# Optimization experiments

Hardware: AMD Instinct MI355X
Metric: run time of the kernel (lower is better)

## Reference

```python
import jax, jax.numpy as jnp
import numpy as np

B, T, D, H, E = 4, 2048, 1024, 4096, 8


def setup_inputs() -> dict:
    key = jax.random.key(0)
    ks = jax.random.split(key, 7)
    x = jax.random.normal(ks[0], (B, T, D), dtype=jnp.float32)
    # Gate: Linear(D, E)
    Wg = jax.random.normal(ks[1], (D, E), dtype=jnp.float32) / np.sqrt(D)
    bg = jax.random.normal(ks[2], (E,), dtype=jnp.float32) * 0.01
    # Experts: E x [Linear(D,H), ReLU, Linear(H,D)] (dropout inactive at eval)
    W1 = jax.random.normal(ks[3], (E, D, H), dtype=jnp.float32) / np.sqrt(D)
    b1 = jax.random.normal(ks[4], (E, H), dtype=jnp.float32) * 0.01
    W2 = jax.random.normal(ks[5], (E, H, D), dtype=jnp.float32) / np.sqrt(H)
    b2 = jax.random.normal(ks[6], (E, D), dtype=jnp.float32) * 0.01
    return {"x": x, "Wg": Wg, "bg": bg, "W1": W1, "b1": b1, "W2": W2, "b2": b2}


def reference(x, Wg, bg, W1, b1, W2, b2):
    # Gate + hard top-1 routing
    gate_scores = x @ Wg + bg                      # [B,T,E]
    top1 = jnp.argmax(gate_scores, axis=-1)        # [B,T]
    onehot = jax.nn.one_hot(top1, Wg.shape[-1], dtype=x.dtype)  # [B,T,E]
    # Dense: every expert MLP over all tokens (matches original's masked
    # formulation: x*mask == x on selected tokens, output re-masked).
    h = jax.nn.relu(jnp.einsum('btd,edh->beth', x, W1) + b1[None, :, None, :])
    y = jnp.einsum('beth,ehd->betd', h, W2) + b2[None, :, None, :]
    # Masked combine: keep only the token's chosen expert output
    out = jnp.einsum('betd,bte->btd', y, onehot)
    return out
```

## Files before the change

kernel.cpp:

```cpp
#include <hip/hip_runtime.h>
#include <hip/hip_bf16.h>
#include <stdint.h>

#define NTOK 8192
#define DDIM 1024
#define HDIM 4096
#define NEXP 8
#define MAXWL1 48
#define MAXWL2 72
#define FFN1_GRID ((HDIM / 128) * MAXWL1)

typedef __attribute__((ext_vector_type(4))) float f32x4;
typedef __attribute__((ext_vector_type(8))) short s16x8;
typedef __attribute__((ext_vector_type(8))) unsigned short u16x8;

__device__ __forceinline__ unsigned short f2bf(float f) {
  union { float f; unsigned int u; } v; v.f = f;
  unsigned int u = v.u;
  u += 0x7FFFu + ((u >> 16) & 1u);
  return (unsigned short)(u >> 16);
}

typedef __attribute__((address_space(3))) unsigned char lds_u8;
typedef const __attribute__((address_space(1))) unsigned char glb_u8;

__device__ __forceinline__ void load_lds16(const void* g, void* l) {
  __builtin_amdgcn_global_load_lds((glb_u8*)g, (lds_u8*)l, 16, 0, 0);
}

__global__ __launch_bounds__(256) void gate_kernel(
    const float* __restrict__ x, const float* __restrict__ Wg,
    const float* __restrict__ bg, int* __restrict__ counts,
    int* __restrict__ lists) {
  const int lane = threadIdx.x & 63;
  const int tok = blockIdx.x * 4 + (threadIdx.x >> 6);
  const float* xr = x + (size_t)tok * DDIM;
  double acc[NEXP];
#pragma unroll
  for (int e = 0; e < NEXP; ++e) acc[e] = 0.0;
#pragma unroll 4
  for (int it = 0; it < DDIM / 64; ++it) {
    const int d = it * 64 + lane;
    const float xv = xr[d];
    const f32x4 w0 = *(const f32x4*)(Wg + (size_t)d * NEXP);
    const f32x4 w1 = *(const f32x4*)(Wg + (size_t)d * NEXP + 4);
#pragma unroll
    for (int j = 0; j < 4; ++j) {
      acc[j]     += (double)xv * (double)w0[j];
      acc[4 + j] += (double)xv * (double)w1[j];
    }
  }
#pragma unroll
  for (int e = 0; e < NEXP; ++e) {
    double v = acc[e];
#pragma unroll
    for (int off = 32; off > 0; off >>= 1) v += __shfl_xor(v, off, 64);
    acc[e] = v;
  }
  if (lane == 0) {
    int best = 0;
    double bv = acc[0] + (double)bg[0];
#pragma unroll
    for (int e = 1; e < NEXP; ++e) {
      const double v = acc[e] + (double)bg[e];
      if (v > bv) { bv = v; best = e; }
    }
    const int pos = atomicAdd(&counts[best], 1);
    lists[best * NTOK + pos] = tok;
  }
}

__global__ void offs_kernel(const int* __restrict__ counts, int* __restrict__ offs,
                            int* __restrict__ wl1, int* __restrict__ wl2) {
  int s = 0;
#pragma unroll
  for (int e = 0; e < NEXP; ++e) { offs[e] = s; s += counts[e]; }
  offs[NEXP] = s;
  int n1 = 0, n2 = 0;
  for (int e = 0; e < NEXP; ++e) {
    const int nb1 = (counts[e] + 255) >> 8;
    for (int b = 0; b < nb1; ++b) wl1[n1++] = (e << 20) | b;
    const int nb2 = (counts[e] + 127) >> 7;
    for (int b = 0; b < nb2; ++b) wl2[n2++] = (e << 20) | b;
  }
  offs[NEXP + 1] = n1;
  offs[NEXP + 2] = n2;
}

__device__ __forceinline__ void transpose_tile(
    const float* __restrict__ ine, unsigned short* __restrict__ oute,
    int R, int C, int c0, int r0, int t, unsigned short* Tb) {
  const int tr = t >> 4, tc4 = (t & 15) * 4;
#pragma unroll
  for (int p = 0; p < 4; ++p) {
    const int r = tr + p * 16;
    const f32x4 v = *(const f32x4*)(ine + (size_t)(r0 + r) * C + c0 + tc4);
#pragma unroll
    for (int j = 0; j < 4; ++j) Tb[r * 66 + tc4 + j] = f2bf(v[j]);
  }
  __syncthreads();
  const int cc = t >> 3, rr8 = (t & 7) * 8;
#pragma unroll
  for (int p = 0; p < 2; ++p) {
    const int c = cc + p * 32;
    u16x8 o;
#pragma unroll
    for (int j = 0; j < 8; ++j) o[j] = Tb[(rr8 + j) * 66 + c];
    *(u16x8*)(oute + (size_t)(c0 + c) * R + r0 + rr8) = o;
  }
}

__global__ __launch_bounds__(256) void transpose_conv_kernel(
    const float* __restrict__ in, unsigned short* __restrict__ out,
    int R, int C) {
  __shared__ __align__(16) unsigned short T[64 * 66];
  const int e = blockIdx.z;
  transpose_tile(in + (size_t)e * R * C, out + (size_t)e * C * R, R, C,
                 blockIdx.x * 64, blockIdx.y * 64, threadIdx.x, T);
}

__global__ __launch_bounds__(512) void gather_w1t_kernel(
    const float* __restrict__ x, const int* __restrict__ offs,
    const int* __restrict__ lists, int* __restrict__ stok,
    unsigned short* __restrict__ xbs, const float* __restrict__ W1,
    unsigned short* __restrict__ Wt1) {
  __shared__ __align__(16) unsigned short TT[2][64 * 66];
  const int bid = blockIdx.x;
  const int tid = threadIdx.x;
  if (bid < NTOK / 8) {
    const int p = bid * 8 + (tid >> 6);
    const int lane = tid & 63;
    int e = 0;
#pragma unroll
    for (int k = 1; k < NEXP; ++k) e += (p >= offs[k]) ? 1 : 0;
    const int tok = lists[e * NTOK + (p - offs[e])];
    if (lane == 0) stok[p] = tok;
    const float* src = x + (size_t)tok * DDIM + lane * 16;
    unsigned short* dst = xbs + (size_t)p * DDIM + lane * 16;
#pragma unroll
    for (int q = 0; q < 2; ++q) {
      const f32x4 a = *(const f32x4*)(src + q * 8);
      const f32x4 b = *(const f32x4*)(src + q * 8 + 4);
      u16x8 o;
#pragma unroll
      for (int j = 0; j < 4; ++j) { o[j] = f2bf(a[j]); o[4 + j] = f2bf(b[j]); }
      *(u16x8*)(dst + q * 8) = o;
    }
  } else {
    const int id = (bid - NTOK / 8) * 2 + (tid >> 8);
    const int t = tid & 255;
    const int e = id >> 10, rem = id & 1023;
    const int cb = rem & 63, rb = rem >> 6;
    transpose_tile(W1 + (size_t)e * DDIM * HDIM, Wt1 + (size_t)e * HDIM * DDIM,
                   DDIM, HDIM, cb * 64, rb * 64, t, TT[tid >> 8]);
  }
}

template <int BM, int BN, int WM, int WN, int K, int N, int MAXWLT,
          bool COLFAST, bool FUSE1>
__device__ __forceinline__ void ffn_body(
    int d, const unsigned short* __restrict__ A,
    const unsigned short* __restrict__ Bt, const float* __restrict__ bias,
    const int* __restrict__ counts, const int* __restrict__ offs,
    const int* __restrict__ wl, const int* __restrict__ stok,
    unsigned short* __restrict__ outb, float* __restrict__ outf, int nwl_idx,
    unsigned short* As0, unsigned short* Bs0,
    unsigned short* As1, unsigned short* Bs1) {
  constexpr int MF = BM / (WM * 16);
  constexpr int NF = BN / (WN * 16);
  constexpr int ISS_A = BM / 128;
  constexpr int ISS_B = BN / 128;
  constexpr int NT = K / 32;
  constexpr int NCB = N / BN;
  constexpr int NWG = NCB * MAXWLT;
  static_assert((NWG & 7) == 0 && (NT & 1) == 0 && NT >= 4, "");
  static_assert(WM * WN == 8, "8 waves");

  const int logical = (d & 7) * (NWG / 8) + (d >> 3);
  int cb, wli;
  if constexpr (COLFAST) { cb = logical % NCB; wli = logical / NCB; }
  else                   { cb = logical / MAXWLT; wli = logical % MAXWLT; }
  if (wli >= offs[nwl_idx]) return;
  const int col0 = cb * BN;
  const int wle = wl[wli];
  const int e = wle >> 20;
  const int bx = wle & 0xFFFFF;
  const int cnt = counts[e];
  const int row0 = offs[e] + bx * BM;

  const int tid = threadIdx.x;
  const int lane = tid & 63;
  const int w = tid >> 6;
  const int wm = w / WN;
  const int wn = w % WN;
  const int fr = lane & 15;
  const int fj = lane >> 4;

  const int swsrc = ((tid & 3) ^ ((tid >> 3) & 3)) * 8;
  const int rb = tid >> 2;
  const unsigned short* srcA[ISS_A];
#pragma unroll
  for (int i = 0; i < ISS_A; ++i) {
    int gr = row0 + i * 128 + rb;
    if (gr > NTOK - 1) gr = NTOK - 1;
    srcA[i] = A + (size_t)gr * K + swsrc;
  }
  const unsigned short* Bte = Bt + (size_t)e * N * K;
  const unsigned short* srcB[ISS_B];
#pragma unroll
  for (int i = 0; i < ISS_B; ++i)
    srcB[i] = Bte + (size_t)(col0 + i * 128 + rb) * K + swsrc;

  const int js = (fj ^ ((fr >> 1) & 3)) * 8;

  f32x4 acc[MF][NF];
#pragma unroll
  for (int m = 0; m < MF; ++m)
#pragma unroll
    for (int n = 0; n < NF; ++n) acc[m][n] = f32x4{0.f, 0.f, 0.f, 0.f};

  auto stage = [&](unsigned short* dA, unsigned short* dB, int kel) {
#pragma unroll
    for (int i = 0; i < ISS_A; ++i)
      load_lds16(srcA[i] + kel, dA + i * 4096 + tid * 8);
#pragma unroll
    for (int i = 0; i < ISS_B; ++i)
      load_lds16(srcB[i] + kel, dB + i * 4096 + tid * 8);
  };

  auto phase = [&](const unsigned short* pA, const unsigned short* pB,
                   unsigned short* nA, unsigned short* nB, int knext,
                   bool do_stage) {
    asm volatile("s_waitcnt vmcnt(0)" ::: "memory");
    __builtin_amdgcn_s_barrier();
    asm volatile("" ::: "memory");
    s16x8 af[MF], bf[NF];
#pragma unroll
    for (int m = 0; m < MF; ++m)
      af[m] = *(const s16x8*)(pA + (wm * MF * 16 + m * 16 + fr) * 32 + js);
#pragma unroll
    for (int n = 0; n < NF; ++n)
      bf[n] = *(const s16x8*)(pB + (wn * NF * 16 + n * 16 + fr) * 32 + js);
    if (do_stage) stage(nA, nB, knext);
    __builtin_amdgcn_s_setprio(1);
#pragma unroll
    for (int m = 0; m < MF; ++m)
#pragma unroll
      for (int n = 0; n < NF; ++n)
        acc[m][n] = __builtin_amdgcn_mfma_f32_16x16x32_bf16(af[m], bf[n],
                                                            acc[m][n], 0, 0, 0);
    __builtin_amdgcn_s_setprio(0);
  };

  stage(As0, Bs0, 0);
#pragma unroll 1
  for (int t = 0; t < NT - 2; t += 2) {
    phase(As0, Bs0, As1, Bs1, (t + 1) * 32, true);
    phase(As1, Bs1, As0, Bs0, (t + 2) * 32, true);
  }
  phase(As0, Bs0, As1, Bs1, (NT - 1) * 32, true);
  phase(As1, Bs1, nullptr, nullptr, 0, false);

#pragma unroll
  for (int n = 0; n < NF; ++n) {
    const int col = col0 + wn * NF * 16 + n * 16 + fr;
    const float bv = bias[e * N + col];
#pragma unroll
    for (int m = 0; m < MF; ++m) {
#pragma unroll
      for (int j = 0; j < 4; ++j) {
        const int rl = wm * MF * 16 + m * 16 + fj * 4 + j;
        if (bx * BM + rl < cnt) {
          if constexpr (FUSE1) {
            outb[(size_t)(row0 + rl) * N + col] = f2bf(fmaxf(acc[m][n][j] + bv, 0.f));
          } else {
            outf[(size_t)stok[row0 + rl] * N + col] = acc[m][n][j] + bv;
          }
        }
      }
    }
  }
}

__global__ __launch_bounds__(512, 4) void ffn1_w2t_kernel(
    const unsigned short* __restrict__ A, const unsigned short* __restrict__ Bt,
    const float* __restrict__ bias, const int* __restrict__ counts,
    const int* __restrict__ offs, const int* __restrict__ wl,
    const int* __restrict__ stok, unsigned short* __restrict__ Hs,
    const float* __restrict__ W2, unsigned short* __restrict__ Wt2) {
  __shared__ __align__(16) unsigned short As0[256 * 32], Bs0[128 * 32];
  __shared__ __align__(16) unsigned short As1[256 * 32], Bs1[128 * 32];
  const int bid = blockIdx.x;
  if (bid < FFN1_GRID) {
    ffn_body<256, 128, 4, 2, DDIM, HDIM, MAXWL1, false, true>(
        bid, A, Bt, bias, counts, offs, wl, stok, Hs, nullptr, NEXP + 1,
        As0, Bs0, As1, Bs1);
  } else {
    const int id = (bid - FFN1_GRID) * 2 + (threadIdx.x >> 8);
    const int t = threadIdx.x & 255;
    const int e = id >> 10, rem = id & 1023;
    const int cb = rem & 15, rb = rem >> 4;
    transpose_tile(W2 + (size_t)e * HDIM * DDIM, Wt2 + (size_t)e * DDIM * HDIM,
                   HDIM, DDIM, cb * 64, rb * 64, t,
                   (threadIdx.x >= 256) ? As1 : As0);
  }
}

template <int BM, int BN, int WM, int WN, int K, int N, int MAXWLT,
          bool COLFAST, bool FUSE1>
__global__ __launch_bounds__(512, 4) void ffn_kernel(
    const unsigned short* __restrict__ A, const unsigned short* __restrict__ Bt,
    const float* __restrict__ bias, const int* __restrict__ counts,
    const int* __restrict__ offs, const int* __restrict__ wl,
    const int* __restrict__ stok, unsigned short* __restrict__ outb,
    float* __restrict__ outf, int nwl_idx) {
  __shared__ __align__(16) unsigned short As0[BM * 32], Bs0[BN * 32];
  __shared__ __align__(16) unsigned short As1[BM * 32], Bs1[BN * 32];
  ffn_body<BM, BN, WM, WN, K, N, MAXWLT, COLFAST, FUSE1>(
      blockIdx.x, A, Bt, bias, counts, offs, wl, stok, outb, outf, nwl_idx,
      As0, Bs0, As1, Bs1);
}

extern "C" void kernel_launch(void* const* d_in, const int* in_sizes, int n_in,
                              void* d_out, int out_size, void* d_ws, size_t ws_size,
                              hipStream_t stream) {
  (void)in_sizes; (void)n_in; (void)out_size;
  const float* x  = (const float*)d_in[0];
  const float* Wg = (const float*)d_in[1];
  const float* bg = (const float*)d_in[2];
  const float* W1 = (const float*)d_in[3];
  const float* b1 = (const float*)d_in[4];
  const float* W2 = (const float*)d_in[5];
  const float* b2 = (const float*)d_in[6];
  float* out = (float*)d_out;

  char* ws = (char*)d_ws;
  const size_t OFF_CNT = 0;
  const size_t OFF_OFF = 128;
  const size_t OFF_WL1 = 256;
  const size_t OFF_WL2 = 256 + MAXWL1 * 4;
  const size_t OFF_LST = 1024;
  const size_t OFF_STK = OFF_LST + (size_t)NEXP * NTOK * 4;
  const size_t OFF_XBS = OFF_STK + (size_t)NTOK * 4;
  const size_t OFF_HS  = OFF_XBS + (size_t)NTOK * DDIM * 2;
  const size_t OFF_WT1 = OFF_HS + (size_t)NTOK * HDIM * 2;
  const size_t SZ_W    = (size_t)NEXP * DDIM * HDIM * 2;
  const size_t OFF_WT2 = OFF_WT1 + SZ_W;
  const size_t NEED_SMALL = OFF_WT1 + SZ_W;
  const size_t NEED_BIG   = OFF_WT2 + SZ_W;
  if (ws_size < NEED_SMALL) return;
  const bool big = (ws_size >= NEED_BIG);

  int* counts = (int*)(ws + OFF_CNT);
  int* offs   = (int*)(ws + OFF_OFF);
  int* wl1    = (int*)(ws + OFF_WL1);
  int* wl2    = (int*)(ws + OFF_WL2);
  int* lists  = (int*)(ws + OFF_LST);
  int* stok   = (int*)(ws + OFF_STK);
  unsigned short* xbs = (unsigned short*)(ws + OFF_XBS);
  unsigned short* Hs  = (unsigned short*)(ws + OFF_HS);
  unsigned short* Wt1 = (unsigned short*)(ws + OFF_WT1);
  unsigned short* Wt2 = big ? (unsigned short*)(ws + OFF_WT2) : Wt1;

  hipMemsetAsync(counts, 0, 128, stream);
  gate_kernel<<<NTOK / 4, 256, 0, stream>>>(x, Wg, bg, counts, lists);
  offs_kernel<<<1, 1, 0, stream>>>(counts, offs, wl1, wl2);

  gather_w1t_kernel<<<NTOK / 8 + 4096, 512, 0, stream>>>(
      x, offs, lists, stok, xbs, W1, Wt1);

  if (big) {
    ffn1_w2t_kernel<<<FFN1_GRID + 4096, 512, 0, stream>>>(
        xbs, Wt1, b1, counts, offs, wl1, stok, Hs, W2, Wt2);
  } else {
    ffn_kernel<256, 128, 4, 2, DDIM, HDIM, MAXWL1, false, true>
        <<<dim3(FFN1_GRID), 512, 0, stream>>>(
            xbs, Wt1, b1, counts, offs, wl1, stok, Hs, nullptr, NEXP + 1);
    transpose_conv_kernel<<<dim3(DDIM / 64, HDIM / 64, NEXP), 256, 0, stream>>>(
        W2, Wt1, HDIM, DDIM);
  }
  ffn_kernel<128, 256, 2, 4, HDIM, DDIM, MAXWL2, true, false>
      <<<dim3((DDIM / 256) * MAXWL2), 512, 0, stream>>>(
          Hs, Wt2, b2, counts, offs, wl2, stok, nullptr, out, NEXP + 2);
}
```

Baseline: 434.0 us.

## Fuse gate routing with W1 transpose and compute offsets in last gate block

Moves the gate computation into the same launch as the W1 transpose/bf16 conversion, so routing overlaps with the weight conversion instead of running as its own kernel. The offsets and worklists are built by whichever gate block finishes last, using an atomic completion counter, which removes the single-thread offs kernel launch. The token gather and bf16 conversion move into a separate kernel after that launch. This trades two small launches for one extra gather launch, and it relies on atomic-counter ordering across blocks being visible without an explicit memory fence.

```diff
diff --git a/kernel.cpp b/kernel.cpp
--- a/kernel.cpp
+++ b/kernel.cpp
@@ -9,6 +9,7 @@
 #define MAXWL1 48
 #define MAXWL2 72
 #define FFN1_GRID ((HDIM / 128) * MAXWL1)
+#define NGATE (NTOK / 8)
 
 typedef __attribute__((ext_vector_type(4))) float f32x4;
 typedef __attribute__((ext_vector_type(8))) short s16x8;
@@ -28,12 +29,10 @@
   __builtin_amdgcn_global_load_lds((glb_u8*)g, (lds_u8*)l, 16, 0, 0);
 }
 
-__global__ __launch_bounds__(256) void gate_kernel(
+__device__ __forceinline__ void gate_wave(
     const float* __restrict__ x, const float* __restrict__ Wg,
     const float* __restrict__ bg, int* __restrict__ counts,
-    int* __restrict__ lists) {
-  const int lane = threadIdx.x & 63;
-  const int tok = blockIdx.x * 4 + (threadIdx.x >> 6);
+    int* __restrict__ lists, int tok, int lane) {
   const float* xr = x + (size_t)tok * DDIM;
   double acc[NEXP];
 #pragma unroll
@@ -70,21 +69,38 @@
   }
 }
 
-__global__ void offs_kernel(const int* __restrict__ counts, int* __restrict__ offs,
-                            int* __restrict__ wl1, int* __restrict__ wl2) {
+__global__ __launch_bounds__(256) void gate_kernel(
+    const float* __restrict__ x, const float* __restrict__ Wg,
+    const float* __restrict__ bg, int* __restrict__ counts,
+    int* __restrict__ lists) {
+  gate_wave(x, Wg, bg, counts, lists, blockIdx.x * 4 + (threadIdx.x >> 6),
+            threadIdx.x & 63);
+}
+
+__device__ __forceinline__ void compute_offs(
+    const int* cnt, int* __restrict__ offs, int* __restrict__ wl1,
+    int* __restrict__ wl2) {
   int s = 0;
 #pragma unroll
-  for (int e = 0; e < NEXP; ++e) { offs[e] = s; s += counts[e]; }
+  for (int e = 0; e < NEXP; ++e) { offs[e] = s; s += cnt[e]; }
   offs[NEXP] = s;
   int n1 = 0, n2 = 0;
   for (int e = 0; e < NEXP; ++e) {
-    const int nb1 = (counts[e] + 255) >> 8;
+    const int nb1 = (cnt[e] + 255) >> 8;
     for (int b = 0; b < nb1; ++b) wl1[n1++] = (e << 20) | b;
-    const int nb2 = (counts[e] + 127) >> 7;
+    const int nb2 = (cnt[e] + 127) >> 7;
     for (int b = 0; b < nb2; ++b) wl2[n2++] = (e << 20) | b;
   }
   offs[NEXP + 1] = n1;
   offs[NEXP + 2] = n2;
+}
+
+__global__ void offs_kernel(const int* __restrict__ counts, int* __restrict__ offs,
+                            int* __restrict__ wl1, int* __restrict__ wl2) {
+  int c[NEXP];
+#pragma unroll
+  for (int e = 0; e < NEXP; ++e) c[e] = counts[e];
+  compute_offs(c, offs, wl1, wl2);
 }
 
 __device__ __forceinline__ void transpose_tile(
@@ -119,40 +135,58 @@
                  blockIdx.x * 64, blockIdx.y * 64, threadIdx.x, T);
 }
 
-__global__ __launch_bounds__(512) void gather_w1t_kernel(
-    const float* __restrict__ x, const int* __restrict__ offs,
-    const int* __restrict__ lists, int* __restrict__ stok,
-    unsigned short* __restrict__ xbs, const float* __restrict__ W1,
-    unsigned short* __restrict__ Wt1) {
+__global__ __launch_bounds__(512) void gate_w1t_kernel(
+    const float* __restrict__ x, const float* __restrict__ Wg,
+    const float* __restrict__ bg, int* __restrict__ counts,
+    int* __restrict__ lists, int* __restrict__ doneCnt,
+    int* __restrict__ offs, int* __restrict__ wl1, int* __restrict__ wl2,
+    const float* __restrict__ W1, unsigned short* __restrict__ Wt1) {
   __shared__ __align__(16) unsigned short TT[2][64 * 66];
   const int bid = blockIdx.x;
   const int tid = threadIdx.x;
-  if (bid < NTOK / 8) {
-    const int p = bid * 8 + (tid >> 6);
-    const int lane = tid & 63;
-    int e = 0;
-#pragma unroll
-    for (int k = 1; k < NEXP; ++k) e += (p >= offs[k]) ? 1 : 0;
-    const int tok = lists[e * NTOK + (p - offs[e])];
-    if (lane == 0) stok[p] = tok;
-    const float* src = x + (size_t)tok * DDIM + lane * 16;
-    unsigned short* dst = xbs + (size_t)p * DDIM + lane * 16;
-#pragma unroll
-    for (int q = 0; q < 2; ++q) {
-      const f32x4 a = *(const f32x4*)(src + q * 8);
-      const f32x4 b = *(const f32x4*)(src + q * 8 + 4);
-      u16x8 o;
-#pragma unroll
-      for (int j = 0; j < 4; ++j) { o[j] = f2bf(a[j]); o[4 + j] = f2bf(b[j]); }
-      *(u16x8*)(dst + q * 8) = o;
+  if (bid < NGATE) {
+    gate_wave(x, Wg, bg, counts, lists, bid * 8 + (tid >> 6), tid & 63);
+    __syncthreads();
+    if (tid == 0) {
+      const int d = atomicAdd(doneCnt, 1);
+      if (d == NGATE - 1) {
+        int c[NEXP];
+#pragma unroll
+        for (int e = 0; e < NEXP; ++e) c[e] = atomicAdd(&counts[e], 0);
+        compute_offs(c, offs, wl1, wl2);
+      }
     }
   } else {
-    const int id = (bid - NTOK / 8) * 2 + (tid >> 8);
+    const int id = (bid - NGATE) * 2 + (tid >> 8);
     const int t = tid & 255;
     const int e = id >> 10, rem = id & 1023;
     const int cb = rem & 63, rb = rem >> 6;
     transpose_tile(W1 + (size_t)e * DDIM * HDIM, Wt1 + (size_t)e * HDIM * DDIM,
                    DDIM, HDIM, cb * 64, rb * 64, t, TT[tid >> 8]);
+  }
+}
+
+__global__ __launch_bounds__(256) void gather_conv_kernel(
+    const float* __restrict__ x, const int* __restrict__ offs,
+    const int* __restrict__ lists, int* __restrict__ stok,
+    unsigned short* __restrict__ xbs) {
+  const int p = blockIdx.x * 4 + (threadIdx.x >> 6);
+  const int lane = threadIdx.x & 63;
+  int e = 0;
+#pragma unroll
+  for (int k = 1; k < NEXP; ++k) e += (p >= offs[k]) ? 1 : 0;
+  const int tok = lists[e * NTOK + (p - offs[e])];
+  if (lane == 0) stok[p] = tok;
+  const float* src = x + (size_t)tok * DDIM + lane * 16;
+  unsigned short* dst = xbs + (size_t)p * DDIM + lane * 16;
+#pragma unroll
+  for (int q = 0; q < 2; ++q) {
+    const f32x4 a = *(const f32x4*)(src + q * 8);
+    const f32x4 b = *(const f32x4*)(src + q * 8 + 4);
+    u16x8 o;
+#pragma unroll
+    for (int j = 0; j < 4; ++j) { o[j] = f2bf(a[j]); o[4 + j] = f2bf(b[j]); }
+    *(u16x8*)(dst + q * 8) = o;
   }
 }
 
@@ -336,6 +370,7 @@
 
   char* ws = (char*)d_ws;
   const size_t OFF_CNT = 0;
+  const size_t OFF_DONE = 64;
   const size_t OFF_OFF = 128;
   const size_t OFF_WL1 = 256;
   const size_t OFF_WL2 = 256 + MAXWL1 * 4;
@@ -352,6 +387,7 @@
   const bool big = (ws_size >= NEED_BIG);
 
   int* counts = (int*)(ws + OFF_CNT);
+  int* doneCnt = (int*)(ws + OFF_DONE);
   int* offs   = (int*)(ws + OFF_OFF);
   int* wl1    = (int*)(ws + OFF_WL1);
   int* wl2    = (int*)(ws + OFF_WL2);
@@ -362,17 +398,20 @@
   unsigned short* Wt1 = (unsigned short*)(ws + OFF_WT1);
   unsigned short* Wt2 = big ? (unsigned short*)(ws + OFF_WT2) : Wt1;
 
-  hipMemsetAsync(counts, 0, 128, stream);
-  gate_kernel<<<NTOK / 4, 256, 0, stream>>>(x, Wg, bg, counts, lists);
-  offs_kernel<<<1, 1, 0, stream>>>(counts, offs, wl1, wl2);
-
-  gather_w1t_kernel<<<NTOK / 8 + 4096, 512, 0, stream>>>(
-      x, offs, lists, stok, xbs, W1, Wt1);
+  hipMemsetAsync(ws, 0, 128, stream);
 
   if (big) {
+    gate_w1t_kernel<<<NGATE + 4096, 512, 0, stream>>>(
+        x, Wg, bg, counts, lists, doneCnt, offs, wl1, wl2, W1, Wt1);
+    gather_conv_kernel<<<NTOK / 4, 256, 0, stream>>>(x, offs, lists, stok, xbs);
     ffn1_w2t_kernel<<<FFN1_GRID + 4096, 512, 0, stream>>>(
         xbs, Wt1, b1, counts, offs, wl1, stok, Hs, W2, Wt2);
   } else {
+    gate_kernel<<<NTOK / 4, 256, 0, stream>>>(x, Wg, bg, counts, lists);
+    offs_kernel<<<1, 1, 0, stream>>>(counts, offs, wl1, wl2);
+    gather_conv_kernel<<<NTOK / 4, 256, 0, stream>>>(x, offs, lists, stok, xbs);
+    transpose_conv_kernel<<<dim3(HDIM / 64, DDIM / 64, NEXP), 256, 0, stream>>>(
+        W1, Wt1, DDIM, HDIM);
     ffn_kernel<256, 128, 4, 2, DDIM, HDIM, MAXWL1, false, true>
         <<<dim3(FFN1_GRID), 512, 0, stream>>>(
             xbs, Wt1, b1, counts, offs, wl1, stok, Hs, nullptr, NEXP + 1);
```

New measurement: 442.3 us. Within noise of the previous version (+1.9%).
